# Kernel tuning notes

Hardware: AMD Instinct MI355X
Metric: run time of the kernel (lower is better)

## Reference

```python
import jax, jax.numpy as jnp
import numpy as np

NUM_HEADS = 8
C = 512


def setup_inputs() -> dict:
    key = jax.random.key(0)
    ks = jax.random.split(key, 8)
    B, D, H, W = 1, 16, 16, 16
    x = jax.random.normal(ks[0], (B, C, D, H, W), dtype=jnp.float32)
    s = 1.0 / np.sqrt(C)
    Wq = jax.random.normal(ks[1], (C, C), dtype=jnp.float32) * s
    Wk = jax.random.normal(ks[2], (C, C), dtype=jnp.float32) * s
    Wv = jax.random.normal(ks[3], (C, C), dtype=jnp.float32) * s
    bq = jax.random.normal(ks[4], (C,), dtype=jnp.float32) * 0.01
    bk = jax.random.normal(ks[5], (C,), dtype=jnp.float32) * 0.01
    bv = jax.random.normal(ks[6], (C,), dtype=jnp.float32) * 0.01
    # torch inits gamma to 0; use 0.5 so the attention branch contributes
    gamma = jnp.full((1,), 0.5, dtype=jnp.float32)
    return {"x": x, "Wq": Wq, "bq": bq, "Wk": Wk, "bk": bk, "Wv": Wv, "bv": bv, "gamma": gamma}


def _attn(x, Wq, bq, Wk, bk, Wv, bv, gamma):
    B, Cc, D, H, W = x.shape
    nh = NUM_HEADS
    hd = Cc // nh
    N = D * H * W

    def proj(Wm, bm):
        # 1x1x1 Conv3d == channel GEMM
        y = jnp.einsum('oc,bcdhw->bodhw', Wm, x) + bm[None, :, None, None, None]
        y = y.reshape(B, nh, hd, D, H, W)            # [B, nh, hd, D, H, W]
        y = jnp.moveaxis(y, 2, -1)                    # [B, nh, D, H, W, hd]
        return y.reshape(B * nh, N, hd)               # [B*nh, N, hd]

    q = proj(Wq, bq)
    k = proj(Wk, bk)
    v = proj(Wv, bv)

    # NOTE: original module has NO 1/sqrt(head_dim) scaling -- faithful.
    energy = jnp.einsum('bnd,bmd->bnm', q, k)         # [B*nh, N, N]
    attention = jax.nn.softmax(energy, axis=-1)
    out = jnp.einsum('bnm,bmd->bnd', attention, v)    # [B*nh, N, hd]

    # Faithful (buggy-in-original) reshape: [B, N, nh, hd] row-major into [B, C, D, H, W]
    out = out.reshape(B, nh, N, hd).transpose(0, 2, 1, 3).reshape(B, Cc, D, H, W)
    return gamma[0] * out + x


def reference(x, Wq, bq, Wk, bk, Wv, bv, gamma):
    return _attn(x, Wq, bq, Wk, bk, Wv, bv, gamma)
```

## Files before the change

### kernel.cpp

```cpp
#include <hip/hip_runtime.h>

typedef unsigned short u16;
typedef __attribute__((ext_vector_type(4))) float f32x4;
typedef __attribute__((ext_vector_type(8))) short s16x8;
typedef __attribute__((ext_vector_type(4))) unsigned short u16x4;
typedef __attribute__((ext_vector_type(8))) unsigned short u16x8;
typedef __attribute__((ext_vector_type(2))) unsigned int u32x2;

#define MFMA(a, b, c) __builtin_amdgcn_mfma_f32_16x16x32_bf16((a), (b), (c), 0, 0, 0)

#define XT_HI 0u
#define XT_LO 2097152u
#define W_HI  4194304u
#define W_LO  4980736u
#define Q_HI  5767168u
#define Q_LO  7864320u
#define K_HI  9961472u
#define K_LO  12058624u
#define V_HI  14155776u
#define V_LO  16252928u
#define WS_BYTES_U16 36700160u

__device__ __forceinline__ u16 f2bf(float f) {
  union { float f; unsigned u; } v; v.f = f;
  unsigned r = v.u + 0x7fffu + ((v.u >> 16) & 1u);
  return (u16)(r >> 16);
}
__device__ __forceinline__ float bf2f(u16 h) {
  union { unsigned u; float f; } v; v.u = ((unsigned)h) << 16;
  return v.f;
}
__device__ __forceinline__ unsigned pk2h(float a, float b) {
  union { float f; unsigned u; } ua, ub; ua.f = a; ub.f = b;
  return __builtin_amdgcn_perm(ub.u + 0x8000u, ua.u + 0x8000u, 0x07060302u);
}
__device__ __forceinline__ void gload16(const void* g, void* l) {
  __builtin_amdgcn_global_load_lds(
      (const __attribute__((address_space(1))) void*)g,
      (__attribute__((address_space(3))) void*)l, 16, 0, 0);
}

__global__ __launch_bounds__(256) void prep_w(const float* __restrict__ wq,
                                              const float* __restrict__ wk,
                                              const float* __restrict__ wv,
                                              u16* __restrict__ ws) {
  unsigned t = blockIdx.x * 256u + threadIdx.x;
  unsigned idx = t * 4u;
  unsigned which = idx >> 18;
  unsigned rem = idx & 262143u;
  const float* src = (which == 0) ? wq : (which == 1) ? wk : wv;
  f32x4 v = *(const f32x4*)(src + rem);
  u16x4 h;
#pragma unroll
  for (int i = 0; i < 4; ++i) h[i] = f2bf(v[i]);
  *(u16x4*)(ws + W_HI + idx) = h;
}

__global__ __launch_bounds__(256) void prep_xt(const float* __restrict__ x,
                                               u16* __restrict__ ws) {
  __shared__ float tile[64][65];
  unsigned t = threadIdx.x;
  unsigned n0 = blockIdx.x * 64u, c0 = blockIdx.y * 64u;
  unsigned cl = t >> 2, ns = (t & 3u) * 16u;
  const float* src = x + (c0 + cl) * 4096u + n0 + ns;
#pragma unroll
  for (int j = 0; j < 16; j += 4) {
    f32x4 v = *(const f32x4*)(src + j);
#pragma unroll
    for (int e = 0; e < 4; ++e) tile[cl][ns + j + e] = v[e];
  }
  __syncthreads();
  unsigned nl = t >> 2, cs = (t & 3u) * 16u;
  u16x8 vh0, vh1, vl0, vl1;
#pragma unroll
  for (int j = 0; j < 16; ++j) {
    float v = tile[cs + j][nl];
    u16 hb = f2bf(v);
    u16 lb = f2bf(v - bf2f(hb));
    if (j < 8) { vh0[j] = hb; vl0[j] = lb; }
    else       { vh1[j - 8] = hb; vl1[j - 8] = lb; }
  }
  unsigned off = (n0 + nl) * 512u + c0 + cs;
  *(u16x8*)(ws + XT_HI + off) = vh0;
  *(u16x8*)(ws + XT_HI + off + 8u) = vh1;
  *(u16x8*)(ws + XT_LO + off) = vl0;
  *(u16x8*)(ws + XT_LO + off + 8u) = vl1;
}

__global__ __launch_bounds__(256) void proj(const float* __restrict__ bq,
                                            const float* __restrict__ bk,
                                            const float* __restrict__ bv,
                                            u16* __restrict__ ws) {
  extern __shared__ u16 sm[];
  const unsigned t = threadIdx.x, w = t >> 6, lane = t & 63u;
  const unsigned g4 = lane >> 4, c = lane & 15u;
  const unsigned z = blockIdx.z;
  const unsigned m0 = blockIdx.y * 64u, n0 = blockIdx.x * 128u;
  const unsigned wo = w >> 1, wn = w & 1u;

  const u16* WHp = ws + W_HI + z * 262144u;
  const u16* XH = ws + XT_HI;
  const u16* XL = ws + XT_LO;

  f32x4 acc[2][4];
#pragma unroll
  for (int a = 0; a < 2; ++a)
#pragma unroll
    for (int b = 0; b < 4; ++b) acc[a][b] = (f32x4){0.f, 0.f, 0.f, 0.f};

  const unsigned r_l = lane >> 2;
  const unsigned cl_ = lane & 3u;

  auto stage = [&](unsigned b, unsigned it) {
    unsigned k0 = it * 32u;
#pragma unroll
    for (unsigned j = 0; j < 5u; ++j) {
      unsigned s = w * 5u + j;
      unsigned sl, dbase, rowoff; const u16* base;
      if (s < 4u)       { sl = s;       dbase = 0u;    base = WHp; rowoff = m0; }
      else if (s < 12u) { sl = s - 4u;  dbase = 2048u; base = XH;  rowoff = n0; }
      else              { sl = s - 12u; dbase = 6144u; base = XL;  rowoff = n0; }
      unsigned r = 16u * sl + r_l;
      unsigned cg = cl_ ^ ((r >> 1) & 3u);
      gload16(base + (rowoff + r) * 512u + k0 + 8u * cg,
              sm + b * 10240u + dbase + sl * 512u);
    }
  };

  auto body = [&](unsigned kb) {
    s16x8 ah[2];
#pragma unroll
    for (int mr = 0; mr < 2; ++mr) {
      unsigned row = 32u * wo + 16u * mr + c;
      unsigned idx = kb + row * 32u + ((g4 ^ ((row >> 1) & 3u)) * 8u);
      ah[mr] = *(const s16x8*)(sm + idx);
    }
#pragma unroll
    for (int nr = 0; nr < 4; ++nr) {
      unsigned row = 64u * wn + 16u * nr + c;
      unsigned idx = kb + 2048u + row * 32u + ((g4 ^ ((row >> 1) & 3u)) * 8u);
      s16x8 bh = *(const s16x8*)(sm + idx);
      s16x8 bl = *(const s16x8*)(sm + idx + 4096u);
#pragma unroll
      for (int mr = 0; mr < 2; ++mr) {
        acc[mr][nr] = MFMA(ah[mr], bh, acc[mr][nr]);
        acc[mr][nr] = MFMA(ah[mr], bl, acc[mr][nr]);
      }
    }
  };

  stage(0u, 0u);
  __syncthreads();
  for (unsigned it = 0; it < 8u; ++it) {
    stage(1u, 2u * it + 1u);
    body(0u);
    __syncthreads();
    if (it < 7u) stage(0u, 2u * it + 2u);
    body(10240u);
    __syncthreads();
  }

  const float* bias = (z == 0) ? bq : (z == 1) ? bk : bv;
  const unsigned obase = m0 + 32u * wo;
#pragma unroll
  for (int mr = 0; mr < 2; ++mr) {
    f32x4 b4 = *(const f32x4*)(bias + obase + 16u * mr + 4u * g4);
#pragma unroll
    for (int nr = 0; nr < 4; ++nr) {
      unsigned n = n0 + 64u * wn + 16u * nr + c;
      float v4[4];
#pragma unroll
      for (int i = 0; i < 4; ++i) v4[i] = acc[mr][nr][i] + b4[i];
      if (z == 0u) {
        unsigned d0 = 32u * wo + 16u * mr + 4u * g4;
        unsigned off = (blockIdx.y * 4096u + n) * 64u + d0;
        u16x4 h4, l4;
#pragma unroll
        for (int i = 0; i < 4; ++i) {
          u16 hb = f2bf(v4[i]);
          h4[i] = hb;
          l4[i] = f2bf(v4[i] - bf2f(hb));
        }
        *(u16x4*)(ws + Q_HI + off) = h4;
        *(u16x4*)(ws + Q_LO + off) = l4;
      } else if (z == 1u) {
        unsigned d0 = 32u * wo + 16u * mr + 4u * g4;
        unsigned off = (blockIdx.y * 4096u + n) * 64u + d0;
        u16x4 h4;
#pragma unroll
        for (int i = 0; i < 4; ++i) h4[i] = f2bf(v4[i]);
        *(u16x4*)(ws + K_HI + off) = h4;
      } else {
#pragma unroll
        for (int i = 0; i < 4; ++i) {
          unsigned o = obase + 16u * mr + 4u * g4 + i;
          ws[V_HI + o * 4096u + n] = f2bf(v4[i]);
        }
      }
    }
  }
}

__global__ __launch_bounds__(256) void attn(const u16* __restrict__ ws,
                                            float* __restrict__ ows,
                                            float* __restrict__ lws) {
  extern __shared__ u16 sm[];
  const unsigned t = threadIdx.x, w = t >> 6, lane = t & 63u;
  const unsigned g4 = lane >> 4, c = lane & 15u;
  const unsigned h = blockIdx.y, sp = blockIdx.z;
  const unsigned q0 = blockIdx.x * 64u;

  const u16* QHp = ws + Q_HI; const u16* QLp = ws + Q_LO;
  const u16* KHp = ws + K_HI;
  const u16* VHp = ws + V_HI;

  s16x8 qh[2], ql[2];
#pragma unroll
  for (int ks = 0; ks < 2; ++ks) {
    unsigned q = q0 + 16u * w + c;
    unsigned off = (h * 4096u + q) * 64u + 8u * g4 + 32u * ks;
    qh[ks] = *(const s16x8*)(QHp + off);
    ql[ks] = *(const s16x8*)(QLp + off);
  }

  f32x4 O[4];
#pragma unroll
  for (int b = 0; b < 4; ++b) O[b] = (f32x4){0.f, 0.f, 0.f, 0.f};
  float lr = 0.f;

  const unsigned r_l = lane >> 3, cl_ = lane & 7u;
  u16* Pw = sm + 16384u + w * 1024u;

  unsigned kidx[2][4], poff[4], paoff[2];
#pragma unroll
  for (int ks = 0; ks < 2; ++ks) {
#pragma unroll
    for (int nr = 0; nr < 4; ++nr) {
      unsigned row = 16u * nr + c;
      kidx[ks][nr] = row * 64u + (((g4 + 4u * ks) ^ (row & 7u)) * 8u);
    }
    paoff[ks] = c * 64u + (((g4 + 4u * ks) ^ (c & 7u)) * 8u);
  }
#pragma unroll
  for (int nr = 0; nr < 4; ++nr)
    poff[nr] = c * 64u + (((2u * nr + (g4 >> 1)) ^ (c & 7u)) * 8u) + (g4 & 1u) * 4u;

  auto stage = [&](unsigned b, unsigned ch) {
    unsigned n0 = sp * 2048u + ch * 64u;
#pragma unroll
    for (unsigned j = 0; j < 4u; ++j) {
      unsigned s = w * 4u + j;
      unsigned pl = s >> 3, sl = s & 7u;
      unsigned r = 8u * sl + r_l;
      unsigned cg = cl_ ^ (r & 7u);
      const u16* gsrc;
      if (pl == 0u) gsrc = KHp + (h * 4096u + n0 + r) * 64u + 8u * cg;
      else          gsrc = VHp + (h * 64u + r) * 4096u + n0 + 8u * cg;
      gload16(gsrc, sm + b * 8192u + pl * 4096u + sl * 512u);
    }
  };

  auto body = [&](unsigned kb) {
    f32x4 S[4];
#pragma unroll
    for (int b = 0; b < 4; ++b) S[b] = (f32x4){0.f, 0.f, 0.f, 0.f};
#pragma unroll
    for (int ks = 0; ks < 2; ++ks)
#pragma unroll
      for (int nr = 0; nr < 4; ++nr) {
        s16x8 kh = *(const s16x8*)(sm + kb + kidx[ks][nr]);
        S[nr] = MFMA(kh, qh[ks], S[nr]);
        S[nr] = MFMA(kh, ql[ks], S[nr]);
      }
    float ls = 0.f;
#pragma unroll
    for (int nr = 0; nr < 4; ++nr) {
      f32x4 s = S[nr];
      float p0 = __expf(s[0] - 40.0f);
      float p1 = __expf(s[1] - 40.0f);
      float p2 = __expf(s[2] - 40.0f);
      float p3 = __expf(s[3] - 40.0f);
      ls += (p0 + p1) + (p2 + p3);
      u32x2 pv;
      pv[0] = pk2h(p0, p1);
      pv[1] = pk2h(p2, p3);
      *(u32x2*)(Pw + poff[nr]) = pv;
    }
    ls += __shfl_xor(ls, 16);
    ls += __shfl_xor(ls, 32);
    lr += ls;
#pragma unroll
    for (int ks = 0; ks < 2; ++ks) {
      s16x8 pa = *(const s16x8*)(Pw + paoff[ks]);
#pragma unroll
      for (int nr = 0; nr < 4; ++nr) {
        s16x8 vh = *(const s16x8*)(sm + kb + 4096u + kidx[ks][nr]);
        O[nr] = MFMA(pa, vh, O[nr]);
      }
    }
  };

  stage(0u, 0u);
  __syncthreads();
  for (unsigned it = 0; it < 16u; ++it) {
    stage(1u, 2u * it + 1u);
    body(0u);
    __syncthreads();
    if (it < 15u) stage(0u, 2u * it + 2u);
    body(8192u);
    __syncthreads();
  }

#pragma unroll
  for (int i = 0; i < 4; ++i) {
    unsigned n = q0 + 16u * w + 4u * g4 + i;
    unsigned lwi = (sp * 8u + h) * 4096u + n;
#pragma unroll
    for (int nr = 0; nr < 4; ++nr)
      ows[lwi * 64u + 16u * nr + c] = O[nr][i];
  }
  if (lane < 16u)
    lws[(sp * 8u + h) * 4096u + q0 + 16u * w + lane] = lr;
}

__global__ __launch_bounds__(256) void combine(const float* __restrict__ x,
                                               const float* __restrict__ gamma,
                                               const float* __restrict__ ows,
                                               const float* __restrict__ lws,
                                               float* __restrict__ out) {
  unsigned t = blockIdx.x * 256u + threadIdx.x;
  unsigned L = t * 4u;
  unsigned n = L >> 9, hd6 = L & 511u, h = hd6 >> 6, d = L & 63u;
  unsigned i0 = (h * 4096u + n) * 64u + d;
  unsigned i1 = ((8u + h) * 4096u + n) * 64u + d;
  f32x4 a = *(const f32x4*)(ows + i0);
  f32x4 b = *(const f32x4*)(ows + i1);
  float l = lws[h * 4096u + n] + lws[(8u + h) * 4096u + n];
  float gi = gamma[0] / l;
  f32x4 xv = *(const f32x4*)(x + L);
  f32x4 r = (a + b) * gi + xv;
  *(f32x4*)(out + L) = r;
}

extern "C" void kernel_launch(void* const* d_in, const int* in_sizes, int n_in,
                              void* d_out, int out_size, void* d_ws, size_t ws_size,
                              hipStream_t stream) {
  const float* x = (const float*)d_in[0];
  const float* wq = (const float*)d_in[1];
  const float* bq = (const float*)d_in[2];
  const float* wk = (const float*)d_in[3];
  const float* bk = (const float*)d_in[4];
  const float* wv = (const float*)d_in[5];
  const float* bv = (const float*)d_in[6];
  const float* gamma = (const float*)d_in[7];
  u16* ws = (u16*)d_ws;
  float* ows = (float*)((char*)d_ws + WS_BYTES_U16);
  float* lws = ows + 4194304u;
  float* out = (float*)d_out;

  prep_w<<<dim3(768), dim3(256), 0, stream>>>(wq, wk, wv, ws);
  prep_xt<<<dim3(64, 8), dim3(256), 0, stream>>>(x, ws);
  (void)hipFuncSetAttribute((const void*)proj,
                            hipFuncAttributeMaxDynamicSharedMemorySize, 40960);
  proj<<<dim3(32, 8, 3), dim3(256), 40960, stream>>>(bq, bk, bv, ws);
  (void)hipFuncSetAttribute((const void*)attn,
                            hipFuncAttributeMaxDynamicSharedMemorySize, 40960);
  attn<<<dim3(64, 8, 2), dim3(256), 40960, stream>>>(ws, ows, lws);
  combine<<<dim3(2048), dim3(256), 0, stream>>>(x, gamma, ows, lws, out);
}
```

Baseline: 174.2 us.

## Compute softmax row sums via MFMA with ones, hoist staging addresses, set priorities

Drops the per-iteration scalar sum of exponentials and its cross-lane shuffles. The row sum is instead accumulated by an extra MFMA of the bf16 probability tile against a vector of ones, and one shuffle-based extraction runs at the end. Staging address computation is hoisted out of the loop into per-thread pointers that advance by a fixed stride. s_setprio brackets the MFMA phases to favour matrix issue. The sum now uses the rounded bf16 probabilities, which changes numerics slightly but keeps them consistent with the P·V product.

```diff
diff --git a/kernel.cpp b/kernel.cpp
--- a/kernel.cpp
+++ b/kernel.cpp
@@ -223,10 +223,15 @@
     ql[ks] = *(const s16x8*)(QLp + off);
   }
 
+  const f32x4 zero4 = {0.f, 0.f, 0.f, 0.f};
+  s16x8 ones;
+#pragma unroll
+  for (int i = 0; i < 8; ++i) ones[i] = (short)0x3F80;
+
   f32x4 O[4];
 #pragma unroll
-  for (int b = 0; b < 4; ++b) O[b] = (f32x4){0.f, 0.f, 0.f, 0.f};
-  float lr = 0.f;
+  for (int b = 0; b < 4; ++b) O[b] = zero4;
+  f32x4 Lacc = zero4;
 
   const unsigned r_l = lane >> 3, cl_ = lane & 7u;
   u16* Pw = sm + 16384u + w * 1024u;
@@ -245,68 +250,74 @@
   for (int nr = 0; nr < 4; ++nr)
     poff[nr] = c * 64u + (((2u * nr + (g4 >> 1)) ^ (c & 7u)) * 8u) + (g4 & 1u) * 4u;
 
-  auto stage = [&](unsigned b, unsigned ch) {
-    unsigned n0 = sp * 2048u + ch * 64u;
+  const unsigned pl = w >> 1;
+  const unsigned sl0 = (w * 4u) & 7u;
+  const unsigned stride = pl ? 64u : 4096u;
+  const u16* gp[4];
+  unsigned dst[4];
+#pragma unroll
+  for (unsigned j = 0; j < 4u; ++j) {
+    unsigned sl = sl0 + j;
+    unsigned r = 8u * sl + r_l;
+    unsigned cg = cl_ ^ (r & 7u);
+    dst[j] = pl * 4096u + sl * 512u;
+    gp[j] = pl ? (VHp + (h * 64u + r) * 4096u + sp * 2048u + 8u * cg)
+               : (KHp + (h * 4096u + sp * 2048u + r) * 64u + 8u * cg);
+  }
+
+  auto stage = [&](unsigned b) {
 #pragma unroll
     for (unsigned j = 0; j < 4u; ++j) {
-      unsigned s = w * 4u + j;
-      unsigned pl = s >> 3, sl = s & 7u;
-      unsigned r = 8u * sl + r_l;
-      unsigned cg = cl_ ^ (r & 7u);
-      const u16* gsrc;
-      if (pl == 0u) gsrc = KHp + (h * 4096u + n0 + r) * 64u + 8u * cg;
-      else          gsrc = VHp + (h * 64u + r) * 4096u + n0 + 8u * cg;
-      gload16(gsrc, sm + b * 8192u + pl * 4096u + sl * 512u);
+      gload16(gp[j], sm + b * 8192u + dst[j]);
+      gp[j] += stride;
     }
   };
 
   auto body = [&](unsigned kb) {
     f32x4 S[4];
-#pragma unroll
-    for (int b = 0; b < 4; ++b) S[b] = (f32x4){0.f, 0.f, 0.f, 0.f};
-#pragma unroll
-    for (int ks = 0; ks < 2; ++ks)
-#pragma unroll
-      for (int nr = 0; nr < 4; ++nr) {
-        s16x8 kh = *(const s16x8*)(sm + kb + kidx[ks][nr]);
-        S[nr] = MFMA(kh, qh[ks], S[nr]);
-        S[nr] = MFMA(kh, ql[ks], S[nr]);
-      }
-    float ls = 0.f;
+    __builtin_amdgcn_s_setprio(1);
+#pragma unroll
+    for (int nr = 0; nr < 4; ++nr) {
+      s16x8 kh = *(const s16x8*)(sm + kb + kidx[0][nr]);
+      S[nr] = MFMA(kh, qh[0], zero4);
+      S[nr] = MFMA(kh, ql[0], S[nr]);
+    }
+#pragma unroll
+    for (int nr = 0; nr < 4; ++nr) {
+      s16x8 kh = *(const s16x8*)(sm + kb + kidx[1][nr]);
+      S[nr] = MFMA(kh, qh[1], S[nr]);
+      S[nr] = MFMA(kh, ql[1], S[nr]);
+    }
+    __builtin_amdgcn_s_setprio(0);
 #pragma unroll
     for (int nr = 0; nr < 4; ++nr) {
       f32x4 s = S[nr];
-      float p0 = __expf(s[0] - 40.0f);
-      float p1 = __expf(s[1] - 40.0f);
-      float p2 = __expf(s[2] - 40.0f);
-      float p3 = __expf(s[3] - 40.0f);
-      ls += (p0 + p1) + (p2 + p3);
       u32x2 pv;
-      pv[0] = pk2h(p0, p1);
-      pv[1] = pk2h(p2, p3);
+      pv[0] = pk2h(__expf(s[0] - 40.0f), __expf(s[1] - 40.0f));
+      pv[1] = pk2h(__expf(s[2] - 40.0f), __expf(s[3] - 40.0f));
       *(u32x2*)(Pw + poff[nr]) = pv;
     }
-    ls += __shfl_xor(ls, 16);
-    ls += __shfl_xor(ls, 32);
-    lr += ls;
+    __builtin_amdgcn_s_setprio(1);
 #pragma unroll
     for (int ks = 0; ks < 2; ++ks) {
       s16x8 pa = *(const s16x8*)(Pw + paoff[ks]);
+      Lacc = MFMA(pa, ones, Lacc);
 #pragma unroll
       for (int nr = 0; nr < 4; ++nr) {
         s16x8 vh = *(const s16x8*)(sm + kb + 4096u + kidx[ks][nr]);
         O[nr] = MFMA(pa, vh, O[nr]);
       }
     }
+    __builtin_amdgcn_s_setprio(0);
   };
 
-  stage(0u, 0u);
+  stage(0u);
   __syncthreads();
   for (unsigned it = 0; it < 16u; ++it) {
-    stage(1u, 2u * it + 1u);
+    stage(1u);
     body(0u);
     __syncthreads();
-    if (it < 15u) stage(0u, 2u * it + 2u);
+    if (it < 15u) stage(0u);
     body(8192u);
     __syncthreads();
   }
@@ -319,8 +330,18 @@
     for (int nr = 0; nr < 4; ++nr)
       ows[lwi * 64u + 16u * nr + c] = O[nr][i];
   }
-  if (lane < 16u)
-    lws[(sp * 8u + h) * 4096u + q0 + 16u * w + lane] = lr;
+  {
+    unsigned rr = lane & 15u;
+    int srcl = (int)(16u * (rr >> 2));
+    float t0 = __shfl(Lacc[0], srcl);
+    float t1 = __shfl(Lacc[1], srcl);
+    float t2 = __shfl(Lacc[2], srcl);
+    float t3 = __shfl(Lacc[3], srcl);
+    unsigned sel = rr & 3u;
+    float lv = sel == 0u ? t0 : sel == 1u ? t1 : sel == 2u ? t2 : t3;
+    if (lane < 16u)
+      lws[(sp * 8u + h) * 4096u + q0 + 16u * w + lane] = lv;
+  }
 }
 
 __global__ __launch_bounds__(256) void combine(const float* __restrict__ x,
```

New measurement: 172.8 us. About the same (-0.8%).
